# Kernel optimization log

Measured on AMD Instinct MI355X. Metric: run time of the kernel, lower is better.

Reference implementation:

```python
import jax, jax.numpy as jnp
import numpy as np

T_SCALES = [0.0, 0.25, 0.5, 0.75, 1.0]  # ODEblock time_scales; Euler step per consecutive pair
NUM_ZEROS = 10
BETA = 0.6  # defined in ODEFunc but unused in its forward


def _odefunc(x, x0, adj, alpha, w, d, w2, d2):
    # x: [B, N, T, Fa]; adj: [N, N]; alpha: [N]; w: [Fa, Fa]; d: [Fa]; w2: [T, T]; d2: [T]
    a = jax.nn.sigmoid(alpha)[None, :, None, None]              # [1, N, 1, 1]
    xa = jnp.einsum('ij,kjln->kiln', adj, x)                    # adjacency propagation over nodes
    dc = jnp.clip(d, 0.0, 1.0)
    W = (w * dc) @ w.T                                          # [Fa, Fa]
    # NOTE: faithful to torch source: 'ijkl,mn->ijkm' has NO shared contraction
    # index => xw = (sum_l x) outer (sum_n W) — reproduced exactly.
    xw = jnp.einsum('ijkl,mn->ijkm', x, W)
    d2c = jnp.clip(d2, 0.0, 1.0)
    W2 = (w2 * d2c) @ w2.T                                      # [T, T]
    xw2 = jnp.einsum('ijkl,kn->ijnl', x, W2)                    # temporal mixing
    # f = alpha/2*xa - x + xw - x + xw2 - x + x0
    return a * 0.5 * xa - 3.0 * x + xw + xw2 + x0


def setup_inputs() -> dict:
    key = jax.random.key(0)
    k1, k2 = jax.random.split(key)
    B, N, T, F = 32, 512, 24, 64
    Fa = F + NUM_ZEROS
    x = jax.random.normal(k1, (B, N, T, F), dtype=jnp.float32)
    adj = jax.random.uniform(k2, (N, N), dtype=jnp.float32) / N  # normalized dense adjacency
    alpha = 0.8 * jnp.ones((N,), jnp.float32)                    # nn.Parameter init 0.8*ones
    w = jnp.eye(Fa, dtype=jnp.float32)                           # nn.Parameter init eye
    d = jnp.ones((Fa,), jnp.float32)                             # nn.Parameter init ones
    w2 = jnp.eye(T, dtype=jnp.float32)
    d2 = jnp.ones((T,), jnp.float32)
    return {"x": x, "adj": adj, "alpha": alpha, "w": w, "d": d, "w2": w2, "d2": d2}


def reference(x, adj, alpha, w, d, w2, d2):
    B, N, T, F = x.shape
    if F == 64:
        x_aug = jnp.concatenate(
            [x, jnp.zeros((B, N, T, NUM_ZEROS), dtype=x.dtype)], axis=3)
    else:
        x_aug = x
    x0 = jax.lax.stop_gradient(x_aug)  # set_x0 uses clone().detach()
    # Euler odeint with two time points does one step: z = x + dt * f(x).
    # Original loop restarts from x_aug each iteration, so f is constant.
    f = _odefunc(x_aug, x0, adj, alpha, w, d, w2, d2)
    z = x_aug
    for i in range(len(T_SCALES) - 1):
        dt = T_SCALES[i + 1] - T_SCALES[i]
        z = x_aug + dt * f  # overwrites z each iteration, as in the torch code
    return jax.nn.relu(z)
```

## Files before the change

kernel.cpp:

```cpp
#include <hip/hip_runtime.h>
#include <hip/hip_fp16.h>
#include <cstdint>
#include <cstddef>

#define B_  32
#define N_  512
#define T_  24
#define F_  64
#define FA_ 74
#define NC  1536

typedef __attribute__((ext_vector_type(8))) _Float16 half8;
typedef __attribute__((ext_vector_type(8))) unsigned short ushort8;
typedef __attribute__((ext_vector_type(4))) float floatx4;

#define WS_ADJ 1536
#define WS_XT  132608
#define WS_E0  12715520

#define AS1(p) ((const __attribute__((address_space(1))) void*)(p))
#define AS3(p) ((__attribute__((address_space(3))) void*)(p))

union h2u { _Float16 h; unsigned short u; };

__global__ __launch_bounds__(256) void pk_kernel(
    const float* __restrict__ adj, const float* __restrict__ alpha,
    const float* __restrict__ w, const float* __restrict__ d,
    const float* __restrict__ w2, const float* __restrict__ d2,
    float* __restrict__ ws) {
  int bid = blockIdx.x;
  int tid = threadIdx.x;
  if (bid < 256) {
    _Float16* adjH = (_Float16*)(ws + WS_ADJ);
    int g = (bid * 256 + tid) * 4;
    int row = g >> 9;
    float sc = 0.125f / (1.f + __expf(-alpha[row]));
    float4 v = *(const float4*)&adj[g];
    ushort4 u4; h2u cv;
    cv.h = (_Float16)(sc * v.x); u4.x = cv.u;
    cv.h = (_Float16)(sc * v.y); u4.y = cv.u;
    cv.h = (_Float16)(sc * v.z); u4.z = cv.u;
    cv.h = (_Float16)(sc * v.w); u4.w = cv.u;
    *(ushort4*)&adjH[g] = u4;
  } else {
    __shared__ float cs[FA_];
    if (tid < FA_) {
      float s = 0.f;
      for (int n = 0; n < FA_; ++n) s += w[n * FA_ + tid];
      cs[tid] = s;
    }
    __syncthreads();
    if (tid < FA_) {
      float s = 0.f;
      for (int p = 0; p < FA_; ++p) {
        float dc = fminf(fmaxf(d[p], 0.f), 1.f);
        s += w[tid * FA_ + p] * dc * cs[p];
      }
      ws[tid] = s;
    }
    for (int e = tid; e < T_ * T_; e += 256) {
      int a = e / T_, b = e % T_;
      float s = 0.f;
      for (int p = 0; p < T_; ++p) {
        float dc = fminf(fmaxf(d2[p], 0.f), 1.f);
        s += w2[a * T_ + p] * dc * w2[b * T_ + p];
      }
      ws[128 + e] = s;
    }
  }
}

__global__ __launch_bounds__(256) void transpose_x_kernel(
    const float* __restrict__ x, float* __restrict__ ws) {
  _Float16* xT = (_Float16*)(ws + WS_XT);
  __shared__ float tile[64 * 65];
  int tid = threadIdx.x;
  int b = blockIdx.z;
  int c0 = blockIdx.x * 64;
  int k0 = blockIdx.y * 64;
#pragma unroll
  for (int it = 0; it < 4; ++it) {
    int g = it * 256 + tid;
    int k = g >> 4, c4 = g & 15;
    float4 v = *(const float4*)&x[((size_t)(b * N_ + k0 + k)) * NC + c0 + c4 * 4];
    tile[k * 65 + c4 * 4 + 0] = v.x;
    tile[k * 65 + c4 * 4 + 1] = v.y;
    tile[k * 65 + c4 * 4 + 2] = v.z;
    tile[k * 65 + c4 * 4 + 3] = v.w;
  }
  __syncthreads();
#pragma unroll
  for (int it = 0; it < 4; ++it) {
    int hh = it * 256 + tid;
    int c = hh >> 4, k4 = hh & 15;
    ushort4 u4; h2u cv;
    cv.h = (_Float16)tile[(k4 * 4 + 0) * 65 + c]; u4.x = cv.u;
    cv.h = (_Float16)tile[(k4 * 4 + 1) * 65 + c]; u4.y = cv.u;
    cv.h = (_Float16)tile[(k4 * 4 + 2) * 65 + c]; u4.z = cv.u;
    cv.h = (_Float16)tile[(k4 * 4 + 3) * 65 + c]; u4.w = cv.u;
    *(ushort4*)&xT[((size_t)b * NC + c0 + c) * 512 + k0 + k4 * 4] = u4;
  }
}

__global__ __launch_bounds__(256) void e_kernel(
    const float* __restrict__ x, float* __restrict__ ws, float* __restrict__ out) {
  __shared__ float xs[4 * NC];
  __shared__ unsigned short es[4 * NC];
  __shared__ float Ss[4 * T_];
  int tid = threadIdx.x;
  int blk = blockIdx.x;
  int b = blk >> 7;
  int i0 = (blk & 127) << 2;
  const float* xb = x + (size_t)(b * N_ + i0) * NC;
#pragma unroll
  for (int it = 0; it < 6; ++it) {
    int g = it * 256 + tid;
    *(float4*)&xs[g * 4] = *(const float4*)&xb[g * 4];
  }
  __syncthreads();

  int node = tid >> 6, f = tid & 63;
  float xcol[24];
#pragma unroll
  for (int t = 0; t < 24; ++t) xcol[t] = xs[node * NC + t * 64 + f];

  float S[24];
#pragma unroll
  for (int t = 0; t < 24; ++t) S[t] = xcol[t];
#pragma unroll
  for (int off = 32; off >= 1; off >>= 1) {
#pragma unroll
    for (int t = 0; t < 24; ++t) S[t] += __shfl_xor(S[t], off, 64);
  }
  if ((tid & 63) == 0) {
#pragma unroll
    for (int t = 0; t < 24; ++t) Ss[node * 24 + t] = S[t];
  }

  const float* __restrict__ W2p = ws + 128;
  float rsWf = ws[f];
#pragma unroll
  for (int t = 0; t < 24; ++t) {
    float a = 0.f;
#pragma unroll
    for (int tp = 0; tp < 24; ++tp) a += xcol[tp] * W2p[t * 24 + tp];
    float val = 0.5f * xcol[t] + 0.25f * S[t] * rsWf + 0.25f * a;
    h2u cv; cv.h = (_Float16)val;
    es[node * NC + t * 64 + f] = cv.u;
  }
  __syncthreads();

  _Float16* E0 = (_Float16*)(ws + WS_E0);
  float4* dst = (float4*)(E0 + (size_t)(b * N_ + i0) * NC);
#pragma unroll
  for (int it = 0; it < 3; ++it) {
    int g = it * 256 + tid;
    dst[g] = *(float4*)&es[g * 8];
  }

#pragma unroll
  for (int it = 0; it < 4; ++it) {
    int e2 = it * 256 + tid;
    if (e2 < 960) {
      int nd = e2 / 240;
      int rem = e2 - nd * 240;
      int t = rem / 10;
      int m = rem - t * 10;
      float val = 0.25f * Ss[nd * 24 + t] * ws[64 + m];
      size_t o = ((size_t)(b * N_ + i0 + nd) * T_ + t) * FA_ + 64 + m;
      out[o] = fmaxf(val, 0.f);
    }
  }
}

__global__ __launch_bounds__(256) void gemm_kernel(
    const float* __restrict__ ws, float* __restrict__ out) {
  const _Float16* adjH = (const _Float16*)(ws + WS_ADJ);
  const _Float16* xT   = (const _Float16*)(ws + WS_XT);
  const _Float16* E0   = (const _Float16*)(ws + WS_E0);

  __shared__ __align__(16) char smem[50176];
  _Float16* As = (_Float16*)smem;
  _Float16* Bs = (_Float16*)(smem + 16384);
  float* accS = (float*)smem;
  _Float16* Es = (_Float16*)(smem + 33792);

  int raw = blockIdx.x;
  int nid = (raw & 7) * 192 + (raw >> 3);
  int iq = nid & 3;
  int rest = nid >> 2;
  int cb = rest % 12;
  int b = rest / 12;
  int i0 = iq * 128;
  int c0 = cb * 128;
  int t0 = cb * 2;

  int tid = threadIdx.x;
  int wave = tid >> 6, lane = tid & 63;
  int mw = (wave & 1) * 64, nw = (wave >> 1) * 64;
  int l15 = lane & 15, l4 = lane >> 4;

  floatx4 acc[4][4];
#pragma unroll
  for (int mt = 0; mt < 4; ++mt)
#pragma unroll
    for (int nt = 0; nt < 4; ++nt) acc[mt][nt] = (floatx4){0.f, 0.f, 0.f, 0.f};

  const size_t bC = (size_t)b * NC;
  for (int k0 = 0; k0 < 512; k0 += 64) {
#pragma unroll
    for (int rep = 0; rep < 4; ++rep) {
      int chunk = rep * 256 + tid;
      int r = chunk >> 3;
      int s = chunk & 7;
      int ss = (s ^ (r & 7)) * 8;
      __builtin_amdgcn_global_load_lds(AS1(adjH + (size_t)(i0 + r) * 512 + k0 + ss),
                                       AS3(&As[chunk * 8]), 16, 0, 0);
      __builtin_amdgcn_global_load_lds(AS1(xT + (bC + c0 + r) * 512 + k0 + ss),
                                       AS3(&Bs[chunk * 8]), 16, 0, 0);
    }
    __syncthreads();
#pragma unroll
    for (int ks = 0; ks < 2; ++ks) {
      half8 af[4], bfv[4];
#pragma unroll
      for (int mt = 0; mt < 4; ++mt) {
        int row = mw + mt * 16 + l15;
        int slot = (ks * 4 + l4) ^ (row & 7);
        af[mt] = *(const half8*)&As[row * 64 + slot * 8];
      }
#pragma unroll
      for (int nt = 0; nt < 4; ++nt) {
        int row = nw + nt * 16 + l15;
        int slot = (ks * 4 + l4) ^ (row & 7);
        bfv[nt] = *(const half8*)&Bs[row * 64 + slot * 8];
      }
#pragma unroll
      for (int mt = 0; mt < 4; ++mt)
#pragma unroll
        for (int nt = 0; nt < 4; ++nt)
          acc[mt][nt] = __builtin_amdgcn_mfma_f32_16x16x32_f16(af[mt], bfv[nt], acc[mt][nt], 0, 0, 0);
    }
    __syncthreads();
  }

  const size_t bE = (size_t)b * N_;
  for (int h = 0; h < 2; ++h) {
#pragma unroll
    for (int it = 0; it < 4; ++it) {
      int chunk = it * 256 + tid;
      int row = chunk >> 4;
      int c8 = (chunk & 15) * 8;
      __builtin_amdgcn_global_load_lds(
          AS1(E0 + (bE + i0 + h * 64 + row) * NC + c0 + c8),
          AS3(&Es[chunk * 8]), 16, 0, 0);
    }
    if ((wave & 1) == h) {
#pragma unroll
      for (int mt = 0; mt < 4; ++mt)
#pragma unroll
        for (int nt = 0; nt < 4; ++nt)
#pragma unroll
          for (int r = 0; r < 4; ++r)
            accS[(mt * 16 + l4 * 4 + r) * 132 + nw + nt * 16 + l15] = acc[mt][nt][r];
    }
    __syncthreads();

    {
      int f = tid & 63;
      int rj = tid >> 6;
#pragma unroll
      for (int jj = 0; jj < 16; ++jj) {
        int row = rj + 4 * jj;
        int grow = i0 + h * 64 + row;
        float v0 = accS[row * 132 + f]      + (float)Es[row * 128 + f];
        float v1 = accS[row * 132 + 64 + f] + (float)Es[row * 128 + 64 + f];
        size_t o = (((size_t)(b * N_ + grow)) * T_ + t0) * FA_ + f;
        out[o] = fmaxf(v0, 0.f);
        out[o + FA_] = fmaxf(v1, 0.f);
      }
    }
    __syncthreads();
  }
}

extern "C" void kernel_launch(void* const* d_in, const int* in_sizes, int n_in,
                              void* d_out, int out_size, void* d_ws, size_t ws_size,
                              hipStream_t stream) {
  const float* x     = (const float*)d_in[0];
  const float* adj   = (const float*)d_in[1];
  const float* alpha = (const float*)d_in[2];
  const float* w     = (const float*)d_in[3];
  const float* d     = (const float*)d_in[4];
  const float* w2    = (const float*)d_in[5];
  const float* d2    = (const float*)d_in[6];
  float* out = (float*)d_out;
  float* ws  = (float*)d_ws;

  hipLaunchKernelGGL(pk_kernel, dim3(257), dim3(256), 0, stream,
                     adj, alpha, w, d, w2, d2, ws);
  hipLaunchKernelGGL(transpose_x_kernel, dim3(24, 8, B_), dim3(256), 0, stream, x, ws);
  hipLaunchKernelGGL(e_kernel, dim3(B_ * (N_ / 4)), dim3(256), 0, stream, x, ws, out);
  hipLaunchKernelGGL(gemm_kernel, dim3(1536), dim3(256), 0, stream, ws, out);
}
```

Measured before the change: 357.5 us.

## Fuse elementwise E-term into GEMM epilogue and merge prep kernels

Result: faster. 318.1 us (-11.0%).

```diff
diff --git a/kernel.cpp b/kernel.cpp
--- a/kernel.cpp
+++ b/kernel.cpp
@@ -16,23 +16,53 @@
 
 #define WS_ADJ 1536
 #define WS_XT  132608
-#define WS_E0  12715520
 
 #define AS1(p) ((const __attribute__((address_space(1))) void*)(p))
 #define AS3(p) ((__attribute__((address_space(3))) void*)(p))
 
 union h2u { _Float16 h; unsigned short u; };
 
-__global__ __launch_bounds__(256) void pk_kernel(
-    const float* __restrict__ adj, const float* __restrict__ alpha,
-    const float* __restrict__ w, const float* __restrict__ d,
-    const float* __restrict__ w2, const float* __restrict__ d2,
-    float* __restrict__ ws) {
+__global__ __launch_bounds__(256) void prep_kernel(
+    const float* __restrict__ x, const float* __restrict__ adj,
+    const float* __restrict__ alpha, const float* __restrict__ w,
+    const float* __restrict__ d, const float* __restrict__ w2,
+    const float* __restrict__ d2, float* __restrict__ ws) {
+  __shared__ float tile[64 * 65];
+  __shared__ float cs[FA_];
   int bid = blockIdx.x;
   int tid = threadIdx.x;
-  if (bid < 256) {
+  if (bid < 6144) {
+    _Float16* xT = (_Float16*)(ws + WS_XT);
+    int ct = bid % 24;
+    int kt = (bid / 24) % 8;
+    int b = bid / 192;
+    int c0 = ct * 64;
+    int k0 = kt * 64;
+#pragma unroll
+    for (int it = 0; it < 4; ++it) {
+      int g = it * 256 + tid;
+      int k = g >> 4, c4 = g & 15;
+      float4 v = *(const float4*)&x[((size_t)(b * N_ + k0 + k)) * NC + c0 + c4 * 4];
+      tile[k * 65 + c4 * 4 + 0] = v.x;
+      tile[k * 65 + c4 * 4 + 1] = v.y;
+      tile[k * 65 + c4 * 4 + 2] = v.z;
+      tile[k * 65 + c4 * 4 + 3] = v.w;
+    }
+    __syncthreads();
+#pragma unroll
+    for (int it = 0; it < 4; ++it) {
+      int hh = it * 256 + tid;
+      int c = hh >> 4, k4 = hh & 15;
+      ushort4 u4; h2u cv;
+      cv.h = (_Float16)tile[(k4 * 4 + 0) * 65 + c]; u4.x = cv.u;
+      cv.h = (_Float16)tile[(k4 * 4 + 1) * 65 + c]; u4.y = cv.u;
+      cv.h = (_Float16)tile[(k4 * 4 + 2) * 65 + c]; u4.z = cv.u;
+      cv.h = (_Float16)tile[(k4 * 4 + 3) * 65 + c]; u4.w = cv.u;
+      *(ushort4*)&xT[((size_t)b * NC + c0 + c) * 512 + k0 + k4 * 4] = u4;
+    }
+  } else if (bid < 6400) {
     _Float16* adjH = (_Float16*)(ws + WS_ADJ);
-    int g = (bid * 256 + tid) * 4;
+    int g = ((bid - 6144) * 256 + tid) * 4;
     int row = g >> 9;
     float sc = 0.125f / (1.f + __expf(-alpha[row]));
     float4 v = *(const float4*)&adj[g];
@@ -43,7 +73,6 @@
     cv.h = (_Float16)(sc * v.w); u4.w = cv.u;
     *(ushort4*)&adjH[g] = u4;
   } else {
-    __shared__ float cs[FA_];
     if (tid < FA_) {
       float s = 0.f;
       for (int n = 0; n < FA_; ++n) s += w[n * FA_ + tid];
@@ -70,120 +99,17 @@
   }
 }
 
-__global__ __launch_bounds__(256) void transpose_x_kernel(
-    const float* __restrict__ x, float* __restrict__ ws) {
-  _Float16* xT = (_Float16*)(ws + WS_XT);
-  __shared__ float tile[64 * 65];
-  int tid = threadIdx.x;
-  int b = blockIdx.z;
-  int c0 = blockIdx.x * 64;
-  int k0 = blockIdx.y * 64;
-#pragma unroll
-  for (int it = 0; it < 4; ++it) {
-    int g = it * 256 + tid;
-    int k = g >> 4, c4 = g & 15;
-    float4 v = *(const float4*)&x[((size_t)(b * N_ + k0 + k)) * NC + c0 + c4 * 4];
-    tile[k * 65 + c4 * 4 + 0] = v.x;
-    tile[k * 65 + c4 * 4 + 1] = v.y;
-    tile[k * 65 + c4 * 4 + 2] = v.z;
-    tile[k * 65 + c4 * 4 + 3] = v.w;
-  }
-  __syncthreads();
-#pragma unroll
-  for (int it = 0; it < 4; ++it) {
-    int hh = it * 256 + tid;
-    int c = hh >> 4, k4 = hh & 15;
-    ushort4 u4; h2u cv;
-    cv.h = (_Float16)tile[(k4 * 4 + 0) * 65 + c]; u4.x = cv.u;
-    cv.h = (_Float16)tile[(k4 * 4 + 1) * 65 + c]; u4.y = cv.u;
-    cv.h = (_Float16)tile[(k4 * 4 + 2) * 65 + c]; u4.z = cv.u;
-    cv.h = (_Float16)tile[(k4 * 4 + 3) * 65 + c]; u4.w = cv.u;
-    *(ushort4*)&xT[((size_t)b * NC + c0 + c) * 512 + k0 + k4 * 4] = u4;
-  }
-}
-
-__global__ __launch_bounds__(256) void e_kernel(
-    const float* __restrict__ x, float* __restrict__ ws, float* __restrict__ out) {
-  __shared__ float xs[4 * NC];
-  __shared__ unsigned short es[4 * NC];
-  __shared__ float Ss[4 * T_];
-  int tid = threadIdx.x;
-  int blk = blockIdx.x;
-  int b = blk >> 7;
-  int i0 = (blk & 127) << 2;
-  const float* xb = x + (size_t)(b * N_ + i0) * NC;
-#pragma unroll
-  for (int it = 0; it < 6; ++it) {
-    int g = it * 256 + tid;
-    *(float4*)&xs[g * 4] = *(const float4*)&xb[g * 4];
-  }
-  __syncthreads();
-
-  int node = tid >> 6, f = tid & 63;
-  float xcol[24];
-#pragma unroll
-  for (int t = 0; t < 24; ++t) xcol[t] = xs[node * NC + t * 64 + f];
-
-  float S[24];
-#pragma unroll
-  for (int t = 0; t < 24; ++t) S[t] = xcol[t];
-#pragma unroll
-  for (int off = 32; off >= 1; off >>= 1) {
-#pragma unroll
-    for (int t = 0; t < 24; ++t) S[t] += __shfl_xor(S[t], off, 64);
-  }
-  if ((tid & 63) == 0) {
-#pragma unroll
-    for (int t = 0; t < 24; ++t) Ss[node * 24 + t] = S[t];
-  }
-
-  const float* __restrict__ W2p = ws + 128;
-  float rsWf = ws[f];
-#pragma unroll
-  for (int t = 0; t < 24; ++t) {
-    float a = 0.f;
-#pragma unroll
-    for (int tp = 0; tp < 24; ++tp) a += xcol[tp] * W2p[t * 24 + tp];
-    float val = 0.5f * xcol[t] + 0.25f * S[t] * rsWf + 0.25f * a;
-    h2u cv; cv.h = (_Float16)val;
-    es[node * NC + t * 64 + f] = cv.u;
-  }
-  __syncthreads();
-
-  _Float16* E0 = (_Float16*)(ws + WS_E0);
-  float4* dst = (float4*)(E0 + (size_t)(b * N_ + i0) * NC);
-#pragma unroll
-  for (int it = 0; it < 3; ++it) {
-    int g = it * 256 + tid;
-    dst[g] = *(float4*)&es[g * 8];
-  }
-
-#pragma unroll
-  for (int it = 0; it < 4; ++it) {
-    int e2 = it * 256 + tid;
-    if (e2 < 960) {
-      int nd = e2 / 240;
-      int rem = e2 - nd * 240;
-      int t = rem / 10;
-      int m = rem - t * 10;
-      float val = 0.25f * Ss[nd * 24 + t] * ws[64 + m];
-      size_t o = ((size_t)(b * N_ + i0 + nd) * T_ + t) * FA_ + 64 + m;
-      out[o] = fmaxf(val, 0.f);
-    }
-  }
-}
-
 __global__ __launch_bounds__(256) void gemm_kernel(
-    const float* __restrict__ ws, float* __restrict__ out) {
+    const float* __restrict__ ws, const float* __restrict__ x,
+    float* __restrict__ out) {
   const _Float16* adjH = (const _Float16*)(ws + WS_ADJ);
   const _Float16* xT   = (const _Float16*)(ws + WS_XT);
-  const _Float16* E0   = (const _Float16*)(ws + WS_E0);
-
-  __shared__ __align__(16) char smem[50176];
+
+  __shared__ __align__(16) char smem[33792];
   _Float16* As = (_Float16*)smem;
   _Float16* Bs = (_Float16*)(smem + 16384);
   float* accS = (float*)smem;
-  _Float16* Es = (_Float16*)(smem + 33792);
+  __shared__ float coefs[48];
 
   int raw = blockIdx.x;
   int nid = (raw & 7) * 192 + (raw >> 3);
@@ -200,6 +126,13 @@
   int mw = (wave & 1) * 64, nw = (wave >> 1) * 64;
   int l15 = lane & 15, l4 = lane >> 4;
 
+  if (tid < 48) {
+    int tl = tid / 24, tp = tid - (tid / 24) * 24;
+    float cf = 0.25f * ws[128 + (t0 + tl) * 24 + tp];
+    if (tp == t0 + tl) cf += 0.5f;
+    coefs[tid] = cf;
+  }
+
   floatx4 acc[4][4];
 #pragma unroll
   for (int mt = 0; mt < 4; ++mt)
@@ -244,17 +177,12 @@
     __syncthreads();
   }
 
-  const size_t bE = (size_t)b * N_;
+  const size_t bN = (size_t)b * N_;
+  int f = tid & 63;
+  int rj = tid >> 6;
+  float rsWf = ws[f];
+  float rsWa = (f < 10) ? ws[64 + f] : 0.f;
   for (int h = 0; h < 2; ++h) {
-#pragma unroll
-    for (int it = 0; it < 4; ++it) {
-      int chunk = it * 256 + tid;
-      int row = chunk >> 4;
-      int c8 = (chunk & 15) * 8;
-      __builtin_amdgcn_global_load_lds(
-          AS1(E0 + (bE + i0 + h * 64 + row) * NC + c0 + c8),
-          AS3(&Es[chunk * 8]), 16, 0, 0);
-    }
     if ((wave & 1) == h) {
 #pragma unroll
       for (int mt = 0; mt < 4; ++mt)
@@ -266,18 +194,34 @@
     }
     __syncthreads();
 
-    {
-      int f = tid & 63;
-      int rj = tid >> 6;
-#pragma unroll
-      for (int jj = 0; jj < 16; ++jj) {
-        int row = rj + 4 * jj;
-        int grow = i0 + h * 64 + row;
-        float v0 = accS[row * 132 + f]      + (float)Es[row * 128 + f];
-        float v1 = accS[row * 132 + 64 + f] + (float)Es[row * 128 + 64 + f];
-        size_t o = (((size_t)(b * N_ + grow)) * T_ + t0) * FA_ + f;
-        out[o] = fmaxf(v0, 0.f);
-        out[o + FA_] = fmaxf(v1, 0.f);
+#pragma unroll 2
+    for (int jj = 0; jj < 16; ++jj) {
+      int row = rj + 4 * jj;
+      int grow = i0 + h * 64 + row;
+      const float* xr = x + (bN + grow) * NC;
+      float xv[24];
+#pragma unroll
+      for (int tp = 0; tp < 24; ++tp) xv[tp] = xr[tp * 64 + f];
+      float s0 = xv[t0], s1 = xv[t0 + 1];
+#pragma unroll
+      for (int off = 32; off >= 1; off >>= 1) {
+        s0 += __shfl_xor(s0, off, 64);
+        s1 += __shfl_xor(s1, off, 64);
+      }
+      float tm0 = 0.f, tm1 = 0.f;
+#pragma unroll
+      for (int tp = 0; tp < 24; ++tp) {
+        tm0 += coefs[tp] * xv[tp];
+        tm1 += coefs[24 + tp] * xv[tp];
+      }
+      float v0 = accS[row * 132 + f]      + tm0 + 0.25f * s0 * rsWf;
+      float v1 = accS[row * 132 + 64 + f] + tm1 + 0.25f * s1 * rsWf;
+      size_t o = ((bN + grow) * T_ + t0) * FA_ + f;
+      out[o] = fmaxf(v0, 0.f);
+      out[o + FA_] = fmaxf(v1, 0.f);
+      if (f < 10) {
+        out[o + 64] = fmaxf(0.25f * s0 * rsWa, 0.f);
+        out[o + FA_ + 64] = fmaxf(0.25f * s1 * rsWa, 0.f);
       }
     }
     __syncthreads();
@@ -297,9 +241,7 @@
   float* out = (float*)d_out;
   float* ws  = (float*)d_ws;
 
-  hipLaunchKernelGGL(pk_kernel, dim3(257), dim3(256), 0, stream,
-                     adj, alpha, w, d, w2, d2, ws);
-  hipLaunchKernelGGL(transpose_x_kernel, dim3(24, 8, B_), dim3(256), 0, stream, x, ws);
-  hipLaunchKernelGGL(e_kernel, dim3(B_ * (N_ / 4)), dim3(256), 0, stream, x, ws, out);
-  hipLaunchKernelGGL(gemm_kernel, dim3(1536), dim3(256), 0, stream, ws, out);
+  hipLaunchKernelGGL(prep_kernel, dim3(6401), dim3(256), 0, stream,
+                     x, adj, alpha, w, d, w2, d2, ws);
+  hipLaunchKernelGGL(gemm_kernel, dim3(1536), dim3(256), 0, stream, ws, x, out);
 }
```

## Merge prep kernels and move elementwise epilogue after GEMM into finish kernel

Applied to the files above, without the earlier changes.

New measurement: 325.2 us. -9.0%, faster.

```diff
diff --git a/kernel.cpp b/kernel.cpp
--- a/kernel.cpp
+++ b/kernel.cpp
@@ -16,23 +16,54 @@
 
 #define WS_ADJ 1536
 #define WS_XT  132608
-#define WS_E0  12715520
+#define WS_Y   12715520
 
 #define AS1(p) ((const __attribute__((address_space(1))) void*)(p))
 #define AS3(p) ((__attribute__((address_space(3))) void*)(p))
 
 union h2u { _Float16 h; unsigned short u; };
 
-__global__ __launch_bounds__(256) void pk_kernel(
-    const float* __restrict__ adj, const float* __restrict__ alpha,
-    const float* __restrict__ w, const float* __restrict__ d,
-    const float* __restrict__ w2, const float* __restrict__ d2,
-    float* __restrict__ ws) {
+__global__ __launch_bounds__(256) void prep_kernel(
+    const float* __restrict__ x, const float* __restrict__ adj,
+    const float* __restrict__ alpha, const float* __restrict__ w,
+    const float* __restrict__ d, const float* __restrict__ w2,
+    const float* __restrict__ d2, float* __restrict__ ws) {
+  __shared__ float tile[64 * 65];
+  __shared__ float cs[FA_];
   int bid = blockIdx.x;
   int tid = threadIdx.x;
-  if (bid < 256) {
+  if (bid < 6144) {
+    _Float16* xT = (_Float16*)(ws + WS_XT);
+    int ct = bid % 24;
+    int kt = (bid / 24) % 8;
+    int b = bid / 192;
+    int c0 = ct * 64;
+    int k0 = kt * 64;
+#pragma unroll
+    for (int it = 0; it < 4; ++it) {
+      int g = it * 256 + tid;
+      int k = g >> 4, c4 = g & 15;
+      float4 v = *(const float4*)&x[((size_t)(b * N_ + k0 + k)) * NC + c0 + c4 * 4];
+      tile[k * 65 + c4 * 4 + 0] = v.x;
+      tile[k * 65 + c4 * 4 + 1] = v.y;
+      tile[k * 65 + c4 * 4 + 2] = v.z;
+      tile[k * 65 + c4 * 4 + 3] = v.w;
+    }
+    __syncthreads();
+#pragma unroll
+    for (int it = 0; it < 4; ++it) {
+      int hh = it * 256 + tid;
+      int c = hh >> 4, k4 = hh & 15;
+      ushort4 u4; h2u cv;
+      cv.h = (_Float16)tile[(k4 * 4 + 0) * 65 + c]; u4.x = cv.u;
+      cv.h = (_Float16)tile[(k4 * 4 + 1) * 65 + c]; u4.y = cv.u;
+      cv.h = (_Float16)tile[(k4 * 4 + 2) * 65 + c]; u4.z = cv.u;
+      cv.h = (_Float16)tile[(k4 * 4 + 3) * 65 + c]; u4.w = cv.u;
+      *(ushort4*)&xT[((size_t)b * NC + c0 + c) * 512 + k0 + k4 * 4] = u4;
+    }
+  } else if (bid < 6400) {
     _Float16* adjH = (_Float16*)(ws + WS_ADJ);
-    int g = (bid * 256 + tid) * 4;
+    int g = ((bid - 6144) * 256 + tid) * 4;
     int row = g >> 9;
     float sc = 0.125f / (1.f + __expf(-alpha[row]));
     float4 v = *(const float4*)&adj[g];
@@ -43,7 +74,6 @@
     cv.h = (_Float16)(sc * v.w); u4.w = cv.u;
     *(ushort4*)&adjH[g] = u4;
   } else {
-    __shared__ float cs[FA_];
     if (tid < FA_) {
       float s = 0.f;
       for (int n = 0; n < FA_; ++n) s += w[n * FA_ + tid];
@@ -70,53 +100,127 @@
   }
 }
 
-__global__ __launch_bounds__(256) void transpose_x_kernel(
-    const float* __restrict__ x, float* __restrict__ ws) {
-  _Float16* xT = (_Float16*)(ws + WS_XT);
-  __shared__ float tile[64 * 65];
+__global__ __launch_bounds__(256) void gemm_kernel(
+    float* __restrict__ ws, float* __restrict__ out) {
+  const _Float16* adjH = (const _Float16*)(ws + WS_ADJ);
+  const _Float16* xT   = (const _Float16*)(ws + WS_XT);
+  unsigned short* Yu   = (unsigned short*)(ws + WS_Y);
+
+  __shared__ __align__(16) char smem[33792];
+  _Float16* As = (_Float16*)smem;
+  _Float16* Bs = (_Float16*)(smem + 16384);
+  float* accS = (float*)smem;
+
+  int raw = blockIdx.x;
+  int nid = (raw & 7) * 192 + (raw >> 3);
+  int iq = nid & 3;
+  int rest = nid >> 2;
+  int cb = rest % 12;
+  int b = rest / 12;
+  int i0 = iq * 128;
+  int c0 = cb * 128;
+
   int tid = threadIdx.x;
-  int b = blockIdx.z;
-  int c0 = blockIdx.x * 64;
-  int k0 = blockIdx.y * 64;
-#pragma unroll
-  for (int it = 0; it < 4; ++it) {
-    int g = it * 256 + tid;
-    int k = g >> 4, c4 = g & 15;
-    float4 v = *(const float4*)&x[((size_t)(b * N_ + k0 + k)) * NC + c0 + c4 * 4];
-    tile[k * 65 + c4 * 4 + 0] = v.x;
-    tile[k * 65 + c4 * 4 + 1] = v.y;
-    tile[k * 65 + c4 * 4 + 2] = v.z;
-    tile[k * 65 + c4 * 4 + 3] = v.w;
-  }
-  __syncthreads();
-#pragma unroll
-  for (int it = 0; it < 4; ++it) {
-    int hh = it * 256 + tid;
-    int c = hh >> 4, k4 = hh & 15;
-    ushort4 u4; h2u cv;
-    cv.h = (_Float16)tile[(k4 * 4 + 0) * 65 + c]; u4.x = cv.u;
-    cv.h = (_Float16)tile[(k4 * 4 + 1) * 65 + c]; u4.y = cv.u;
-    cv.h = (_Float16)tile[(k4 * 4 + 2) * 65 + c]; u4.z = cv.u;
-    cv.h = (_Float16)tile[(k4 * 4 + 3) * 65 + c]; u4.w = cv.u;
-    *(ushort4*)&xT[((size_t)b * NC + c0 + c) * 512 + k0 + k4 * 4] = u4;
-  }
-}
-
-__global__ __launch_bounds__(256) void e_kernel(
-    const float* __restrict__ x, float* __restrict__ ws, float* __restrict__ out) {
+  int wave = tid >> 6, lane = tid & 63;
+  int mw = (wave & 1) * 64, nw = (wave >> 1) * 64;
+  int l15 = lane & 15, l4 = lane >> 4;
+
+  floatx4 acc[4][4];
+#pragma unroll
+  for (int mt = 0; mt < 4; ++mt)
+#pragma unroll
+    for (int nt = 0; nt < 4; ++nt) acc[mt][nt] = (floatx4){0.f, 0.f, 0.f, 0.f};
+
+  const size_t bC = (size_t)b * NC;
+  for (int k0 = 0; k0 < 512; k0 += 64) {
+#pragma unroll
+    for (int rep = 0; rep < 4; ++rep) {
+      int chunk = rep * 256 + tid;
+      int r = chunk >> 3;
+      int s = chunk & 7;
+      int ss = (s ^ (r & 7)) * 8;
+      __builtin_amdgcn_global_load_lds(AS1(adjH + (size_t)(i0 + r) * 512 + k0 + ss),
+                                       AS3(&As[chunk * 8]), 16, 0, 0);
+      __builtin_amdgcn_global_load_lds(AS1(xT + (bC + c0 + r) * 512 + k0 + ss),
+                                       AS3(&Bs[chunk * 8]), 16, 0, 0);
+    }
+    __syncthreads();
+#pragma unroll
+    for (int ks = 0; ks < 2; ++ks) {
+      half8 af[4], bfv[4];
+#pragma unroll
+      for (int mt = 0; mt < 4; ++mt) {
+        int row = mw + mt * 16 + l15;
+        int slot = (ks * 4 + l4) ^ (row & 7);
+        af[mt] = *(const half8*)&As[row * 64 + slot * 8];
+      }
+#pragma unroll
+      for (int nt = 0; nt < 4; ++nt) {
+        int row = nw + nt * 16 + l15;
+        int slot = (ks * 4 + l4) ^ (row & 7);
+        bfv[nt] = *(const half8*)&Bs[row * 64 + slot * 8];
+      }
+#pragma unroll
+      for (int mt = 0; mt < 4; ++mt)
+#pragma unroll
+        for (int nt = 0; nt < 4; ++nt)
+          acc[mt][nt] = __builtin_amdgcn_mfma_f32_16x16x32_f16(af[mt], bfv[nt], acc[mt][nt], 0, 0, 0);
+    }
+    __syncthreads();
+  }
+
+  const size_t bN = (size_t)b * N_;
+  int f = tid & 63;
+  int rj = tid >> 6;
+  for (int h = 0; h < 2; ++h) {
+    if ((wave & 1) == h) {
+#pragma unroll
+      for (int mt = 0; mt < 4; ++mt)
+#pragma unroll
+        for (int nt = 0; nt < 4; ++nt)
+#pragma unroll
+          for (int r = 0; r < 4; ++r)
+            accS[(mt * 16 + l4 * 4 + r) * 132 + nw + nt * 16 + l15] = acc[mt][nt][r];
+    }
+    __syncthreads();
+
+#pragma unroll 4
+    for (int jj = 0; jj < 16; ++jj) {
+      int row = rj + 4 * jj;
+      int grow = i0 + h * 64 + row;
+      h2u c0v, c1v;
+      c0v.h = (_Float16)accS[row * 132 + f];
+      c1v.h = (_Float16)accS[row * 132 + 64 + f];
+      size_t yb = (bN + grow) * NC + c0;
+      Yu[yb + f] = c0v.u;
+      Yu[yb + 64 + f] = c1v.u;
+    }
+    __syncthreads();
+  }
+}
+
+__global__ __launch_bounds__(256) void finish_kernel(
+    const float* __restrict__ ws, const float* __restrict__ x,
+    float* __restrict__ out) {
   __shared__ float xs[4 * NC];
-  __shared__ unsigned short es[4 * NC];
+  __shared__ unsigned short Ys[4 * NC];
   __shared__ float Ss[4 * T_];
   int tid = threadIdx.x;
   int blk = blockIdx.x;
   int b = blk >> 7;
   int i0 = (blk & 127) << 2;
   const float* xb = x + (size_t)(b * N_ + i0) * NC;
+  const float4* Yb = (const float4*)((const _Float16*)(ws + WS_Y) + (size_t)(b * N_ + i0) * NC);
 #pragma unroll
   for (int it = 0; it < 6; ++it) {
     int g = it * 256 + tid;
     *(float4*)&xs[g * 4] = *(const float4*)&xb[g * 4];
   }
+#pragma unroll
+  for (int it = 0; it < 3; ++it) {
+    int g = it * 256 + tid;
+    ((float4*)Ys)[g] = Yb[g];
+  }
   __syncthreads();
 
   int node = tid >> 6, f = tid & 63;
@@ -144,19 +248,12 @@
     float a = 0.f;
 #pragma unroll
     for (int tp = 0; tp < 24; ++tp) a += xcol[tp] * W2p[t * 24 + tp];
-    float val = 0.5f * xcol[t] + 0.25f * S[t] * rsWf + 0.25f * a;
-    h2u cv; cv.h = (_Float16)val;
-    es[node * NC + t * 64 + f] = cv.u;
+    h2u cy; cy.u = Ys[node * NC + t * 64 + f];
+    float val = (float)cy.h + 0.5f * xcol[t] + 0.25f * S[t] * rsWf + 0.25f * a;
+    size_t o = ((size_t)(b * N_ + i0 + node) * T_ + t) * FA_ + f;
+    out[o] = fmaxf(val, 0.f);
   }
   __syncthreads();
-
-  _Float16* E0 = (_Float16*)(ws + WS_E0);
-  float4* dst = (float4*)(E0 + (size_t)(b * N_ + i0) * NC);
-#pragma unroll
-  for (int it = 0; it < 3; ++it) {
-    int g = it * 256 + tid;
-    dst[g] = *(float4*)&es[g * 8];
-  }
 
 #pragma unroll
   for (int it = 0; it < 4; ++it) {
@@ -170,117 +267,6 @@
       size_t o = ((size_t)(b * N_ + i0 + nd) * T_ + t) * FA_ + 64 + m;
       out[o] = fmaxf(val, 0.f);
     }
-  }
-}
-
-__global__ __launch_bounds__(256) void gemm_kernel(
-    const float* __restrict__ ws, float* __restrict__ out) {
-  const _Float16* adjH = (const _Float16*)(ws + WS_ADJ);
-  const _Float16* xT   = (const _Float16*)(ws + WS_XT);
-  const _Float16* E0   = (const _Float16*)(ws + WS_E0);
-
-  __shared__ __align__(16) char smem[50176];
-  _Float16* As = (_Float16*)smem;
-  _Float16* Bs = (_Float16*)(smem + 16384);
-  float* accS = (float*)smem;
-  _Float16* Es = (_Float16*)(smem + 33792);
-
-  int raw = blockIdx.x;
-  int nid = (raw & 7) * 192 + (raw >> 3);
-  int iq = nid & 3;
-  int rest = nid >> 2;
-  int cb = rest % 12;
-  int b = rest / 12;
-  int i0 = iq * 128;
-  int c0 = cb * 128;
-  int t0 = cb * 2;
-
-  int tid = threadIdx.x;
-  int wave = tid >> 6, lane = tid & 63;
-  int mw = (wave & 1) * 64, nw = (wave >> 1) * 64;
-  int l15 = lane & 15, l4 = lane >> 4;
-
-  floatx4 acc[4][4];
-#pragma unroll
-  for (int mt = 0; mt < 4; ++mt)
-#pragma unroll
-    for (int nt = 0; nt < 4; ++nt) acc[mt][nt] = (floatx4){0.f, 0.f, 0.f, 0.f};
-
-  const size_t bC = (size_t)b * NC;
-  for (int k0 = 0; k0 < 512; k0 += 64) {
-#pragma unroll
-    for (int rep = 0; rep < 4; ++rep) {
-      int chunk = rep * 256 + tid;
-      int r = chunk >> 3;
-      int s = chunk & 7;
-      int ss = (s ^ (r & 7)) * 8;
-      __builtin_amdgcn_global_load_lds(AS1(adjH + (size_t)(i0 + r) * 512 + k0 + ss),
-                                       AS3(&As[chunk * 8]), 16, 0, 0);
-      __builtin_amdgcn_global_load_lds(AS1(xT + (bC + c0 + r) * 512 + k0 + ss),
-                                       AS3(&Bs[chunk * 8]), 16, 0, 0);
-    }
-    __syncthreads();
-#pragma unroll
-    for (int ks = 0; ks < 2; ++ks) {
-      half8 af[4], bfv[4];
-#pragma unroll
-      for (int mt = 0; mt < 4; ++mt) {
-        int row = mw + mt * 16 + l15;
-        int slot = (ks * 4 + l4) ^ (row & 7);
-        af[mt] = *(const half8*)&As[row * 64 + slot * 8];
-      }
-#pragma unroll
-      for (int nt = 0; nt < 4; ++nt) {
-        int row = nw + nt * 16 + l15;
-        int slot = (ks * 4 + l4) ^ (row & 7);
-        bfv[nt] = *(const half8*)&Bs[row * 64 + slot * 8];
-      }
-#pragma unroll
-      for (int mt = 0; mt < 4; ++mt)
-#pragma unroll
-        for (int nt = 0; nt < 4; ++nt)
-          acc[mt][nt] = __builtin_amdgcn_mfma_f32_16x16x32_f16(af[mt], bfv[nt], acc[mt][nt], 0, 0, 0);
-    }
-    __syncthreads();
-  }
-
-  const size_t bE = (size_t)b * N_;
-  for (int h = 0; h < 2; ++h) {
-#pragma unroll
-    for (int it = 0; it < 4; ++it) {
-      int chunk = it * 256 + tid;
-      int row = chunk >> 4;
-      int c8 = (chunk & 15) * 8;
-      __builtin_amdgcn_global_load_lds(
-          AS1(E0 + (bE + i0 + h * 64 + row) * NC + c0 + c8),
-          AS3(&Es[chunk * 8]), 16, 0, 0);
-    }
-    if ((wave & 1) == h) {
-#pragma unroll
-      for (int mt = 0; mt < 4; ++mt)
-#pragma unroll
-        for (int nt = 0; nt < 4; ++nt)
-#pragma unroll
-          for (int r = 0; r < 4; ++r)
-            accS[(mt * 16 + l4 * 4 + r) * 132 + nw + nt * 16 + l15] = acc[mt][nt][r];
-    }
-    __syncthreads();
-
-    {
-      int f = tid & 63;
-      int rj = tid >> 6;
-#pragma unroll
-      for (int jj = 0; jj < 16; ++jj) {
-        int row = rj + 4 * jj;
-        int grow = i0 + h * 64 + row;
-        float v0 = accS[row * 132 + f]      + (float)Es[row * 128 + f];
-        float v1 = accS[row * 132 + 64 + f] + (float)Es[row * 128 + 64 + f];
-        size_t o = (((size_t)(b * N_ + grow)) * T_ + t0) * FA_ + f;
-        out[o] = fmaxf(v0, 0.f);
-        out[o + FA_] = fmaxf(v1, 0.f);
-      }
-    }
-    __syncthreads();
   }
 }
 
@@ -297,9 +283,8 @@
   float* out = (float*)d_out;
   float* ws  = (float*)d_ws;
 
-  hipLaunchKernelGGL(pk_kernel, dim3(257), dim3(256), 0, stream,
-                     adj, alpha, w, d, w2, d2, ws);
-  hipLaunchKernelGGL(transpose_x_kernel, dim3(24, 8, B_), dim3(256), 0, stream, x, ws);
-  hipLaunchKernelGGL(e_kernel, dim3(B_ * (N_ / 4)), dim3(256), 0, stream, x, ws, out);
+  hipLaunchKernelGGL(prep_kernel, dim3(6401), dim3(256), 0, stream,
+                     x, adj, alpha, w, d, w2, d2, ws);
   hipLaunchKernelGGL(gemm_kernel, dim3(1536), dim3(256), 0, stream, ws, out);
-}
+  hipLaunchKernelGGL(finish_kernel, dim3(B_ * (N_ / 4)), dim3(256), 0, stream, ws, x, out);
+}
```
